# Kernel tuning notes

Measured on AMD Instinct MI355X. Metric: run time of the kernel, lower is better.

## Reference

```python
import jax, jax.numpy as jnp
import numpy as np

UNITS = 1024

def setup_inputs() -> dict:
    key = jax.random.key(0)
    k1, k2, k3 = jax.random.split(key, 3)
    B, T, F = 32, 512, 1024
    scale_g = 1.0 / np.sqrt(F + UNITS)
    return {
        "inputs": jax.random.normal(k1, (B, T, F), dtype=jnp.float32),
        "gate_kernel": jax.random.normal(k2, (F + UNITS, 2 * UNITS), dtype=jnp.float32) * scale_g,
        "gate_bias": jnp.ones((2 * UNITS,), dtype=jnp.float32),  # TF GRUCell default gate bias = 1.0
        "cand_kernel": jax.random.normal(k3, (F + UNITS, UNITS), dtype=jnp.float32) * scale_g,
        "cand_bias": jnp.zeros((UNITS,), dtype=jnp.float32),
    }

def _gru_step(x, h, gate_kernel, gate_bias, cand_kernel, cand_bias):
    # TF GRUCell math: gates from [x, h], candidate from [x, r*h]
    xh = jnp.concatenate([x, h], axis=-1)                      # [B, F+U]
    gates = jax.nn.sigmoid(xh @ gate_kernel + gate_bias)       # [B, 2U]
    r, u = jnp.split(gates, 2, axis=-1)
    xrh = jnp.concatenate([x, r * h], axis=-1)
    c = jnp.tanh(xrh @ cand_kernel + cand_bias)                # [B, U]
    return u * h + (1.0 - u) * c

def reference(inputs, gate_kernel, gate_bias, cand_kernel, cand_bias):
    B = inputs.shape[0]
    h0 = jnp.zeros((B, UNITS), dtype=jnp.float32)  # cell.zero_state
    xs = jnp.swapaxes(inputs, 0, 1)                # [T, B, F] (unstack over time)

    def step(h, x):
        h_new = _gru_step(x, h, gate_kernel, gate_bias, cand_kernel, cand_bias)
        return h_new, h_new  # GRU output == new state

    _, ys = jax.lax.scan(step, h0, xs)             # ys: [T, B, U]
    return jnp.swapaxes(ys, 0, 1)                  # stack on axis=1 -> [B, T, U]
```

## Files before the change

kernel.cpp:

```cpp
#include <hip/hip_runtime.h>
#include <math.h>

#define BB 32
#define TT 512
#define FF 1024
#define UU 1024

typedef __attribute__((ext_vector_type(8))) short s8v;
typedef __attribute__((ext_vector_type(4))) float f4v;

static __device__ __forceinline__ unsigned short f2bf(float f) {
    unsigned int u = __builtin_bit_cast(unsigned int, f);
    u += 0x7fff + ((u >> 16) & 1);
    return (unsigned short)(u >> 16);
}
static __device__ __forceinline__ float bf2f(unsigned short b) {
    unsigned int u = ((unsigned int)b) << 16;
    return __builtin_bit_cast(float, u);
}

__global__ __launch_bounds__(256) void cvt_bf16(
    const float* __restrict__ in, unsigned short* __restrict__ out, int n4)
{
    int i = blockIdx.x * 256 + threadIdx.x;
    if (i < n4) {
        float4 v = ((const float4*)in)[i];
        ushort4 o;
        o.x = f2bf(v.x); o.y = f2bf(v.y); o.z = f2bf(v.z); o.w = f2bf(v.w);
        ((ushort4*)out)[i] = o;
    }
}

template<int ROWS, int COLS>
__global__ __launch_bounds__(256) void transpose_bf16(
    const float* __restrict__ W, unsigned short* __restrict__ WT)
{
    __shared__ float tl[32][33];
    const int tx = threadIdx.x, ty = threadIdx.y;
    const int bx = blockIdx.x, by = blockIdx.y;
    #pragma unroll
    for (int i = 0; i < 4; ++i) {
        int r = by * 32 + ty + i * 8;
        int c = bx * 32 + tx;
        tl[ty + i * 8][tx] = W[(size_t)r * COLS + c];
    }
    __syncthreads();
    #pragma unroll
    for (int i = 0; i < 4; ++i) {
        int n = bx * 32 + ty + i * 8;
        int k = by * 32 + tx;
        WT[(size_t)n * ROWS + k] = f2bf(tl[tx][ty + i * 8]);
    }
}

__global__ __launch_bounds__(256) void gemm_xproj(
    const unsigned short* __restrict__ A,
    const unsigned short* __restrict__ BT,
    unsigned short* __restrict__ C,
    int N)
{
    __shared__ unsigned short Al[128][72];
    __shared__ unsigned short Bl[128][72];
    const int tid  = threadIdx.x;
    const int lane = tid & 63;
    const int wave = tid >> 6;
    const int l15  = lane & 15;
    const int kg   = lane >> 4;
    const int m0   = blockIdx.y * 128;
    const int n0   = blockIdx.x * 128;
    const int rowOff = (wave >> 1) * 64;
    const int colOff = (wave & 1) * 64;

    f4v acc[4][4];
    #pragma unroll
    for (int m = 0; m < 4; ++m)
        #pragma unroll
        for (int n = 0; n < 4; ++n) acc[m][n] = (f4v){0.f, 0.f, 0.f, 0.f};

    for (int k0 = 0; k0 < 1024; k0 += 64) {
        #pragma unroll
        for (int it = 0; it < 4; ++it) {
            int c = tid + it * 256;
            int r = c >> 3, off = (c & 7) * 8;
            *(s8v*)&Al[r][off] = *(const s8v*)(A + (size_t)(m0 + r) * 1024 + k0 + off);
            *(s8v*)&Bl[r][off] = *(const s8v*)(BT + (size_t)(n0 + r) * 2048 + k0 + off);
        }
        __syncthreads();
        #pragma unroll
        for (int ks = 0; ks < 2; ++ks) {
            s8v a[4], b[4];
            #pragma unroll
            for (int m = 0; m < 4; ++m)
                a[m] = *(const s8v*)&Al[rowOff + m * 16 + l15][ks * 32 + kg * 8];
            #pragma unroll
            for (int n = 0; n < 4; ++n)
                b[n] = *(const s8v*)&Bl[colOff + n * 16 + l15][ks * 32 + kg * 8];
            #pragma unroll
            for (int m = 0; m < 4; ++m)
                #pragma unroll
                for (int n = 0; n < 4; ++n)
                    acc[m][n] = __builtin_amdgcn_mfma_f32_16x16x32_bf16(a[m], b[n], acc[m][n], 0, 0, 0);
        }
        __syncthreads();
    }
    #pragma unroll
    for (int m = 0; m < 4; ++m)
        #pragma unroll
        for (int n = 0; n < 4; ++n)
            #pragma unroll
            for (int i = 0; i < 4; ++i) {
                int row = m0 + rowOff + m * 16 + kg * 4 + i;
                int col = n0 + colOff + n * 16 + l15;
                C[(size_t)row * N + col] = f2bf(acc[m][n][i]);
            }
}

__global__ __launch_bounds__(256) void gru_gates2(
    const unsigned short* __restrict__ hb,
    const unsigned short* __restrict__ WgT,
    const unsigned short* __restrict__ Xgb,
    const float* __restrict__ bg,
    const float* __restrict__ h,
    unsigned short* __restrict__ rhb,
    float* __restrict__ ubuf,
    int t)
{
    __shared__ unsigned short hb_l[32][1032];
    __shared__ unsigned short Wl[16][1032];
    __shared__ float red[4][32][16];
    const int tid  = threadIdx.x;
    const int lane = tid & 63;
    const int wave = tid >> 6;
    const int l15  = lane & 15;
    const int kg   = lane >> 4;
    const int j0   = blockIdx.x * 16;

    #pragma unroll
    for (int it = 0; it < 16; ++it) {
        int c = tid + it * 256;
        int r = c >> 7, off = (c & 127) * 8;
        *(s8v*)&hb_l[r][off] = *(const s8v*)(hb + (size_t)r * 1024 + off);
    }
    #pragma unroll
    for (int it = 0; it < 8; ++it) {
        int c = tid + it * 256;
        int r = c >> 7, off = (c & 127) * 8;
        *(s8v*)&Wl[r][off] = *(const s8v*)(WgT + (size_t)(j0 + r) * 2048 + 1024 + off);
    }
    __syncthreads();

    f4v acc0 = (f4v){0.f,0.f,0.f,0.f}, acc1 = (f4v){0.f,0.f,0.f,0.f};
    const int kbase = wave * 256;
    #pragma unroll
    for (int kk = 0; kk < 8; ++kk) {
        int k = kbase + kk * 32 + kg * 8;
        s8v a0 = *(const s8v*)&hb_l[l15][k];
        s8v a1 = *(const s8v*)&hb_l[16 + l15][k];
        s8v b  = *(const s8v*)&Wl[l15][k];
        acc0 = __builtin_amdgcn_mfma_f32_16x16x32_bf16(a0, b, acc0, 0, 0, 0);
        acc1 = __builtin_amdgcn_mfma_f32_16x16x32_bf16(a1, b, acc1, 0, 0, 0);
    }
    #pragma unroll
    for (int i = 0; i < 4; ++i) {
        red[wave][kg * 4 + i][l15]      = acc0[i];
        red[wave][16 + kg * 4 + i][l15] = acc1[i];
    }
    __syncthreads();

    for (int e = tid; e < 512; e += 256) {
        int b = e >> 4, col = e & 15;
        int j = j0 + col;
        float pre = red[0][b][col] + red[1][b][col] + red[2][b][col] + red[3][b][col];
        pre += bf2f(Xgb[((size_t)b * TT + t) * 2048 + j]) + bg[j];
        float s = 1.f / (1.f + __expf(-pre));
        if (j < UU) rhb[b * UU + j] = f2bf(s * h[b * UU + j]);
        else        ubuf[b * UU + (j - UU)] = s;
    }
}

__global__ __launch_bounds__(256) void gru_cand2(
    const unsigned short* __restrict__ rhb,
    const unsigned short* __restrict__ WcT,
    const unsigned short* __restrict__ Xcb,
    const float* __restrict__ bc,
    const float* __restrict__ ubuf,
    float* __restrict__ h,
    unsigned short* __restrict__ hb,
    float* __restrict__ out,
    int t)
{
    __shared__ unsigned short rh_l[32][1032];
    __shared__ unsigned short Wl[16][1032];
    __shared__ float red[4][32][16];
    const int tid  = threadIdx.x;
    const int lane = tid & 63;
    const int wave = tid >> 6;
    const int l15  = lane & 15;
    const int kg   = lane >> 4;
    const int j0   = blockIdx.x * 16;

    #pragma unroll
    for (int it = 0; it < 16; ++it) {
        int c = tid + it * 256;
        int r = c >> 7, off = (c & 127) * 8;
        *(s8v*)&rh_l[r][off] = *(const s8v*)(rhb + (size_t)r * 1024 + off);
    }
    #pragma unroll
    for (int it = 0; it < 8; ++it) {
        int c = tid + it * 256;
        int r = c >> 7, off = (c & 127) * 8;
        *(s8v*)&Wl[r][off] = *(const s8v*)(WcT + (size_t)(j0 + r) * 2048 + 1024 + off);
    }
    __syncthreads();

    f4v acc0 = (f4v){0.f,0.f,0.f,0.f}, acc1 = (f4v){0.f,0.f,0.f,0.f};
    const int kbase = wave * 256;
    #pragma unroll
    for (int kk = 0; kk < 8; ++kk) {
        int k = kbase + kk * 32 + kg * 8;
        s8v a0 = *(const s8v*)&rh_l[l15][k];
        s8v a1 = *(const s8v*)&rh_l[16 + l15][k];
        s8v b  = *(const s8v*)&Wl[l15][k];
        acc0 = __builtin_amdgcn_mfma_f32_16x16x32_bf16(a0, b, acc0, 0, 0, 0);
        acc1 = __builtin_amdgcn_mfma_f32_16x16x32_bf16(a1, b, acc1, 0, 0, 0);
    }
    #pragma unroll
    for (int i = 0; i < 4; ++i) {
        red[wave][kg * 4 + i][l15]      = acc0[i];
        red[wave][16 + kg * 4 + i][l15] = acc1[i];
    }
    __syncthreads();

    for (int e = tid; e < 512; e += 256) {
        int b = e >> 4, col = e & 15;
        int j = j0 + col;
        float pre = red[0][b][col] + red[1][b][col] + red[2][b][col] + red[3][b][col];
        pre += bf2f(Xcb[((size_t)b * TT + t) * 1024 + j]) + bc[j];
        float cv = tanhf(pre);
        float u  = ubuf[b * UU + j];
        float hv = h[b * UU + j];
        float hn = u * hv + (1.f - u) * cv;
        h[b * UU + j]  = hn;
        hb[b * UU + j] = f2bf(hn);
        out[((size_t)b * TT + t) * UU + j] = hn;
    }
}

__global__ __launch_bounds__(256) void gru_gates(
    const float* __restrict__ x, const float* __restrict__ Wg,
    const float* __restrict__ bg, const float* __restrict__ h,
    float* __restrict__ rh, float* __restrict__ ubuf, int t)
{
    __shared__ float xh[BB][64];
    __shared__ float wl[64][32];
    const int tid = threadIdx.x, jloc = tid & 31, b0 = (tid >> 5) * 4;
    const int j0 = blockIdx.x * 32;
    float acc0 = 0.f, acc1 = 0.f, acc2 = 0.f, acc3 = 0.f;
    for (int k0 = 0; k0 < FF + UU; k0 += 64) {
        for (int idx = tid; idx < BB * 64; idx += 256) {
            int b = idx >> 6, kk = idx & 63, k = k0 + kk;
            xh[b][kk] = (k < FF) ? x[(size_t)b * TT * FF + (size_t)t * FF + k]
                                 : h[b * UU + (k - FF)];
        }
        for (int idx = tid; idx < 64 * 32; idx += 256) {
            int kk = idx >> 5, jj = idx & 31;
            wl[kk][jj] = Wg[(size_t)(k0 + kk) * (2 * UU) + (j0 + jj)];
        }
        __syncthreads();
        #pragma unroll
        for (int kk = 0; kk < 64; kk += 4) {
            float w0 = wl[kk][jloc], w1 = wl[kk+1][jloc], w2 = wl[kk+2][jloc], w3 = wl[kk+3][jloc];
            float4 a0 = *(const float4*)&xh[b0+0][kk], a1 = *(const float4*)&xh[b0+1][kk];
            float4 a2 = *(const float4*)&xh[b0+2][kk], a3 = *(const float4*)&xh[b0+3][kk];
            acc0 += a0.x*w0 + a0.y*w1 + a0.z*w2 + a0.w*w3;
            acc1 += a1.x*w0 + a1.y*w1 + a1.z*w2 + a1.w*w3;
            acc2 += a2.x*w0 + a2.y*w1 + a2.z*w2 + a2.w*w3;
            acc3 += a3.x*w0 + a3.y*w1 + a3.z*w2 + a3.w*w3;
        }
        __syncthreads();
    }
    const int j = j0 + jloc;
    const float bias = bg[j];
    float g[4] = {acc0+bias, acc1+bias, acc2+bias, acc3+bias};
    #pragma unroll
    for (int i = 0; i < 4; ++i) {
        int b = b0 + i;
        float s = 1.f / (1.f + expf(-g[i]));
        if (j < UU) rh[b * UU + j] = s * h[b * UU + j];
        else        ubuf[b * UU + (j - UU)] = s;
    }
}

__global__ __launch_bounds__(256) void gru_cand(
    const float* __restrict__ x, const float* __restrict__ Wc,
    const float* __restrict__ bc, const float* __restrict__ rh,
    const float* __restrict__ ubuf, float* __restrict__ h,
    float* __restrict__ out, int t)
{
    __shared__ float xh[BB][64];
    __shared__ float wl[64][32];
    const int tid = threadIdx.x, jloc = tid & 31, b0 = (tid >> 5) * 4;
    const int j0 = blockIdx.x * 32;
    float acc0 = 0.f, acc1 = 0.f, acc2 = 0.f, acc3 = 0.f;
    for (int k0 = 0; k0 < FF + UU; k0 += 64) {
        for (int idx = tid; idx < BB * 64; idx += 256) {
            int b = idx >> 6, kk = idx & 63, k = k0 + kk;
            xh[b][kk] = (k < FF) ? x[(size_t)b * TT * FF + (size_t)t * FF + k]
                                 : rh[b * UU + (k - FF)];
        }
        for (int idx = tid; idx < 64 * 32; idx += 256) {
            int kk = idx >> 5, jj = idx & 31;
            wl[kk][jj] = Wc[(size_t)(k0 + kk) * UU + (j0 + jj)];
        }
        __syncthreads();
        #pragma unroll
        for (int kk = 0; kk < 64; kk += 4) {
            float w0 = wl[kk][jloc], w1 = wl[kk+1][jloc], w2 = wl[kk+2][jloc], w3 = wl[kk+3][jloc];
            float4 a0 = *(const float4*)&xh[b0+0][kk], a1 = *(const float4*)&xh[b0+1][kk];
            float4 a2 = *(const float4*)&xh[b0+2][kk], a3 = *(const float4*)&xh[b0+3][kk];
            acc0 += a0.x*w0 + a0.y*w1 + a0.z*w2 + a0.w*w3;
            acc1 += a1.x*w0 + a1.y*w1 + a1.z*w2 + a1.w*w3;
            acc2 += a2.x*w0 + a2.y*w1 + a2.z*w2 + a2.w*w3;
            acc3 += a3.x*w0 + a3.y*w1 + a3.z*w2 + a3.w*w3;
        }
        __syncthreads();
    }
    const int j = j0 + jloc;
    const float bias = bc[j];
    float cpre[4] = {acc0+bias, acc1+bias, acc2+bias, acc3+bias};
    #pragma unroll
    for (int i = 0; i < 4; ++i) {
        int b = b0 + i;
        float c  = tanhf(cpre[i]);
        float u  = ubuf[b * UU + j];
        float hv = h[b * UU + j];
        float hn = u * hv + (1.f - u) * c;
        h[b * UU + j] = hn;
        out[(size_t)b * TT * UU + (size_t)t * UU + j] = hn;
    }
}

extern "C" void kernel_launch(void* const* d_in, const int* in_sizes, int n_in,
                              void* d_out, int out_size, void* d_ws, size_t ws_size,
                              hipStream_t stream) {
    const float* x  = (const float*)d_in[0];
    const float* Wg = (const float*)d_in[1];
    const float* bg = (const float*)d_in[2];
    const float* Wc = (const float*)d_in[3];
    const float* bc = (const float*)d_in[4];
    float* out = (float*)d_out;

    const size_t XB_B  = (size_t)BB * TT * FF * 2;
    const size_t WGT_B = (size_t)2 * UU * (FF + UU) * 2;
    const size_t WCT_B = (size_t)UU * (FF + UU) * 2;
    const size_t XG_B  = (size_t)BB * TT * 2 * UU * 2;
    const size_t XC_B  = (size_t)BB * TT * UU * 2;
    const size_t H_B   = (size_t)BB * UU * 4;
    const size_t HB_B  = (size_t)BB * UU * 2;
    const size_t NEED  = XB_B + WGT_B + WCT_B + XG_B + XC_B + H_B + HB_B * 2 + H_B;

    if (ws_size >= NEED) {
        char* p = (char*)d_ws;
        unsigned short* xb  = (unsigned short*)p;            p += XB_B;
        unsigned short* WgT = (unsigned short*)p;            p += WGT_B;
        unsigned short* WcT = (unsigned short*)p;            p += WCT_B;
        unsigned short* Xgb = (unsigned short*)p;            p += XG_B;
        unsigned short* Xcb = (unsigned short*)p;            p += XC_B;
        float*          h   = (float*)p;                     p += H_B;
        unsigned short* hb  = (unsigned short*)p;            p += HB_B;
        unsigned short* rhb = (unsigned short*)p;            p += HB_B;
        float*          ub  = (float*)p;                     p += H_B;

        cvt_bf16<<<(BB * TT * FF / 4 + 255) / 256, 256, 0, stream>>>(x, xb, BB * TT * FF / 4);
        transpose_bf16<FF + UU, 2 * UU><<<dim3(64, 64), dim3(32, 8), 0, stream>>>(Wg, WgT);
        transpose_bf16<FF + UU, UU>    <<<dim3(32, 64), dim3(32, 8), 0, stream>>>(Wc, WcT);
        gemm_xproj<<<dim3(2 * UU / 128, BB * TT / 128), 256, 0, stream>>>(xb, WgT, Xgb, 2 * UU);
        gemm_xproj<<<dim3(UU / 128,     BB * TT / 128), 256, 0, stream>>>(xb, WcT, Xcb, UU);
        hipMemsetAsync(h,  0, H_B,  stream);
        hipMemsetAsync(hb, 0, HB_B, stream);

        for (int t = 0; t < TT; ++t) {
            gru_gates2<<<128, 256, 0, stream>>>(hb, WgT, Xgb, bg, h, rhb, ub, t);
            gru_cand2 <<< 64, 256, 0, stream>>>(rhb, WcT, Xcb, bc, ub, h, hb, out, t);
        }
    } else {
        float* h    = (float*)d_ws;
        float* rh   = h  + BB * UU;
        float* ubuf = rh + BB * UU;
        hipMemsetAsync(h, 0, BB * UU * sizeof(float), stream);
        for (int t = 0; t < TT; ++t) {
            gru_gates<<<64, 256, 0, stream>>>(x, Wg, bg, h, rh, ubuf, t);
            gru_cand <<<32, 256, 0, stream>>>(x, Wc, bc, rh, ubuf, h, out, t);
        }
    }
}
```

Measured before the change: 5.307 ms.

## Replace per-timestep kernel launches with persistent kernel using grid barriers

Fuses the gate and candidate recurrent kernels into one persistent kernel of 64 blocks that loops over all 512 timesteps, with an atomic-counter grid barrier between phases. Recurrent weight slices are held in registers across all timesteps instead of being reloaded into shared memory each launch. The aim is to remove about 1024 kernel launches and the repeated weight traffic. In exchange it relies on all 64 blocks being co-resident and spin-waits on global atomics. It also swaps tanhf for a clamped exp-based tanh and drops the fp32 fallback path.

```diff
diff --git a/kernel.cpp b/kernel.cpp
--- a/kernel.cpp
+++ b/kernel.cpp
@@ -5,6 +5,7 @@
 #define TT 512
 #define FF 1024
 #define UU 1024
+#define NBLK 64
 
 typedef __attribute__((ext_vector_type(8))) short s8v;
 typedef __attribute__((ext_vector_type(4))) float f4v;
@@ -115,40 +116,207 @@
             }
 }
 
-__global__ __launch_bounds__(256) void gru_gates2(
-    const unsigned short* __restrict__ hb,
+__device__ __forceinline__ void grid_barrier(unsigned* counter, unsigned* gen,
+                                             unsigned epoch, int tid)
+{
+    __syncthreads();
+    if (tid == 0) {
+        __threadfence();
+        unsigned arrived = __hip_atomic_fetch_add(counter, 1u, __ATOMIC_ACQ_REL,
+                                                  __HIP_MEMORY_SCOPE_AGENT);
+        if (arrived == NBLK - 1) {
+            __hip_atomic_store(counter, 0u, __ATOMIC_RELAXED, __HIP_MEMORY_SCOPE_AGENT);
+            __hip_atomic_store(gen, epoch, __ATOMIC_RELEASE, __HIP_MEMORY_SCOPE_AGENT);
+        } else {
+            while (__hip_atomic_load(gen, __ATOMIC_ACQUIRE, __HIP_MEMORY_SCOPE_AGENT) < epoch)
+                __builtin_amdgcn_s_sleep(1);
+        }
+    }
+    __syncthreads();
+}
+
+__global__ __launch_bounds__(256, 1) void gru_persistent(
     const unsigned short* __restrict__ WgT,
+    const unsigned short* __restrict__ WcT,
     const unsigned short* __restrict__ Xgb,
+    const unsigned short* __restrict__ Xcb,
     const float* __restrict__ bg,
-    const float* __restrict__ h,
+    const float* __restrict__ bc,
+    float* __restrict__ h,
+    unsigned short* __restrict__ hb,
     unsigned short* __restrict__ rhb,
-    float* __restrict__ ubuf,
-    int t)
-{
-    __shared__ unsigned short hb_l[32][1032];
-    __shared__ unsigned short Wl[16][1032];
-    __shared__ float red[4][32][16];
+    float* __restrict__ ub,
+    float* __restrict__ out,
+    unsigned* __restrict__ bar)
+{
+    __shared__ float red[4][32][32];
     const int tid  = threadIdx.x;
     const int lane = tid & 63;
     const int wave = tid >> 6;
     const int l15  = lane & 15;
     const int kg   = lane >> 4;
-    const int j0   = blockIdx.x * 16;
-
+    const int blk  = blockIdx.x;
+    const int gj0  = blk * 32;
+    const int cj0  = blk * 16;
+    const int kb   = wave * 256;
+    const bool is_r = (gj0 < UU);
+
+    s8v bgf[2][8], bcf[8];
+    #pragma unroll
+    for (int n = 0; n < 2; ++n)
+        #pragma unroll
+        for (int kk = 0; kk < 8; ++kk)
+            bgf[n][kk] = *(const s8v*)(WgT + (size_t)(gj0 + n * 16 + l15) * 2048
+                                            + 1024 + kb + kk * 32 + kg * 8);
+    #pragma unroll
+    for (int kk = 0; kk < 8; ++kk)
+        bcf[kk] = *(const s8v*)(WcT + (size_t)(cj0 + l15) * 2048
+                                     + 1024 + kb + kk * 32 + kg * 8);
+
+    const int eb = tid >> 3;
+    const int eq = tid & 7;
+    const float4 bgv = *(const float4*)(bg + gj0 + eq * 4);
+    const float2 bcv = *(const float2*)(bc + cj0 + eq * 2);
+
+    unsigned* counter = bar;
+    unsigned* gen     = bar + 1;
+    unsigned epoch = 0;
+
+    for (int t = 0; t < TT; ++t) {
+        ushort4 xg = *(const ushort4*)(Xgb + ((size_t)eb * TT + t) * 2048 + gj0 + eq * 4);
+        float4 hsl;
+        if (is_r) hsl = *(const float4*)(h + eb * UU + gj0 + eq * 4);
+
+        s8v a[2][8];
+        #pragma unroll
+        for (int m = 0; m < 2; ++m)
+            #pragma unroll
+            for (int kk = 0; kk < 8; ++kk)
+                a[m][kk] = *(const s8v*)(hb + (size_t)(m * 16 + l15) * 1024 + kb + kk * 32 + kg * 8);
+
+        f4v acc[2][2];
+        #pragma unroll
+        for (int m = 0; m < 2; ++m)
+            #pragma unroll
+            for (int n = 0; n < 2; ++n) acc[m][n] = (f4v){0.f, 0.f, 0.f, 0.f};
+        #pragma unroll
+        for (int kk = 0; kk < 8; ++kk)
+            #pragma unroll
+            for (int m = 0; m < 2; ++m)
+                #pragma unroll
+                for (int n = 0; n < 2; ++n)
+                    acc[m][n] = __builtin_amdgcn_mfma_f32_16x16x32_bf16(a[m][kk], bgf[n][kk], acc[m][n], 0, 0, 0);
+
+        #pragma unroll
+        for (int m = 0; m < 2; ++m)
+            #pragma unroll
+            for (int n = 0; n < 2; ++n)
+                #pragma unroll
+                for (int i = 0; i < 4; ++i)
+                    red[wave][m * 16 + kg * 4 + i][n * 16 + l15] = acc[m][n][i];
+        __syncthreads();
+
+        f4v pre = *(const f4v*)&red[0][eb][eq * 4];
+        #pragma unroll
+        for (int w = 1; w < 4; ++w) pre += *(const f4v*)&red[w][eb][eq * 4];
+        pre[0] += bf2f(xg.x) + bgv.x;
+        pre[1] += bf2f(xg.y) + bgv.y;
+        pre[2] += bf2f(xg.z) + bgv.z;
+        pre[3] += bf2f(xg.w) + bgv.w;
+        float s0 = 1.f / (1.f + __expf(-pre[0]));
+        float s1 = 1.f / (1.f + __expf(-pre[1]));
+        float s2 = 1.f / (1.f + __expf(-pre[2]));
+        float s3 = 1.f / (1.f + __expf(-pre[3]));
+        if (is_r) {
+            ushort4 o;
+            o.x = f2bf(s0 * hsl.x); o.y = f2bf(s1 * hsl.y);
+            o.z = f2bf(s2 * hsl.z); o.w = f2bf(s3 * hsl.w);
+            *(ushort4*)(rhb + eb * UU + gj0 + eq * 4) = o;
+        } else {
+            float4 uo = {s0, s1, s2, s3};
+            *(float4*)(ub + eb * UU + (gj0 - UU) + eq * 4) = uo;
+        }
+        ++epoch;
+        grid_barrier(counter, gen, epoch, tid);
+
+        ushort2 xc = *(const ushort2*)(Xcb + ((size_t)eb * TT + t) * 1024 + cj0 + eq * 2);
+        float2 uv  = *(const float2*)(ub + eb * UU + cj0 + eq * 2);
+        float2 hv  = *(const float2*)(h  + eb * UU + cj0 + eq * 2);
+
+        s8v ac[2][8];
+        #pragma unroll
+        for (int m = 0; m < 2; ++m)
+            #pragma unroll
+            for (int kk = 0; kk < 8; ++kk)
+                ac[m][kk] = *(const s8v*)(rhb + (size_t)(m * 16 + l15) * 1024 + kb + kk * 32 + kg * 8);
+
+        f4v acc2[2];
+        acc2[0] = (f4v){0.f, 0.f, 0.f, 0.f};
+        acc2[1] = (f4v){0.f, 0.f, 0.f, 0.f};
+        #pragma unroll
+        for (int kk = 0; kk < 8; ++kk)
+            #pragma unroll
+            for (int m = 0; m < 2; ++m)
+                acc2[m] = __builtin_amdgcn_mfma_f32_16x16x32_bf16(ac[m][kk], bcf[kk], acc2[m], 0, 0, 0);
+
+        float* redc = (float*)red;
+        __syncthreads();
+        #pragma unroll
+        for (int m = 0; m < 2; ++m)
+            #pragma unroll
+            for (int i = 0; i < 4; ++i)
+                redc[((size_t)wave * 32 + m * 16 + kg * 4 + i) * 16 + l15] = acc2[m][i];
+        __syncthreads();
+
+        float2 pre2 = *(const float2*)&redc[(0 * 32 + eb) * 16 + eq * 2];
+        #pragma unroll
+        for (int w = 1; w < 4; ++w) {
+            float2 p = *(const float2*)&redc[((size_t)w * 32 + eb) * 16 + eq * 2];
+            pre2.x += p.x; pre2.y += p.y;
+        }
+        float c0 = pre2.x + bf2f(xc.x) + bcv.x;
+        float c1 = pre2.y + bf2f(xc.y) + bcv.y;
+        c0 = fminf(fmaxf(c0, -15.f), 15.f);
+        c1 = fminf(fmaxf(c1, -15.f), 15.f);
+        float e0 = __expf(2.f * c0), e1 = __expf(2.f * c1);
+        float t0 = (e0 - 1.f) / (e0 + 1.f);
+        float t1 = (e1 - 1.f) / (e1 + 1.f);
+        float hn0 = uv.x * hv.x + (1.f - uv.x) * t0;
+        float hn1 = uv.y * hv.y + (1.f - uv.y) * t1;
+
+        *(float2*)(h + eb * UU + cj0 + eq * 2) = make_float2(hn0, hn1);
+        ushort2 hbo; hbo.x = f2bf(hn0); hbo.y = f2bf(hn1);
+        *(ushort2*)(hb + eb * UU + cj0 + eq * 2) = hbo;
+        *(float2*)(out + ((size_t)eb * TT + t) * UU + cj0 + eq * 2) = make_float2(hn0, hn1);
+
+        ++epoch;
+        grid_barrier(counter, gen, epoch, tid);
+    }
+}
+
+__global__ __launch_bounds__(256) void gru_gates2(
+    const unsigned short* __restrict__ hb, const unsigned short* __restrict__ WgT,
+    const unsigned short* __restrict__ Xgb, const float* __restrict__ bg,
+    const float* __restrict__ h, unsigned short* __restrict__ rhb,
+    float* __restrict__ ubuf, int t)
+{
+    __shared__ unsigned short hb_l[32][1032];
+    __shared__ unsigned short Wl[16][1032];
+    __shared__ float red[4][32][16];
+    const int tid = threadIdx.x, lane = tid & 63, wave = tid >> 6;
+    const int l15 = lane & 15, kg = lane >> 4;
+    const int j0 = blockIdx.x * 16;
     #pragma unroll
     for (int it = 0; it < 16; ++it) {
-        int c = tid + it * 256;
-        int r = c >> 7, off = (c & 127) * 8;
+        int c = tid + it * 256; int r = c >> 7, off = (c & 127) * 8;
         *(s8v*)&hb_l[r][off] = *(const s8v*)(hb + (size_t)r * 1024 + off);
     }
     #pragma unroll
     for (int it = 0; it < 8; ++it) {
-        int c = tid + it * 256;
-        int r = c >> 7, off = (c & 127) * 8;
+        int c = tid + it * 256; int r = c >> 7, off = (c & 127) * 8;
         *(s8v*)&Wl[r][off] = *(const s8v*)(WgT + (size_t)(j0 + r) * 2048 + 1024 + off);
     }
     __syncthreads();
-
     f4v acc0 = (f4v){0.f,0.f,0.f,0.f}, acc1 = (f4v){0.f,0.f,0.f,0.f};
     const int kbase = wave * 256;
     #pragma unroll
@@ -162,11 +330,10 @@
     }
     #pragma unroll
     for (int i = 0; i < 4; ++i) {
-        red[wave][kg * 4 + i][l15]      = acc0[i];
+        red[wave][kg * 4 + i][l15] = acc0[i];
         red[wave][16 + kg * 4 + i][l15] = acc1[i];
     }
     __syncthreads();
-
     for (int e = tid; e < 512; e += 256) {
         int b = e >> 4, col = e & 15;
         int j = j0 + col;
@@ -179,40 +346,28 @@
 }
 
 __global__ __launch_bounds__(256) void gru_cand2(
-    const unsigned short* __restrict__ rhb,
-    const unsigned short* __restrict__ WcT,
-    const unsigned short* __restrict__ Xcb,
-    const float* __restrict__ bc,
-    const float* __restrict__ ubuf,
-    float* __restrict__ h,
-    unsigned short* __restrict__ hb,
-    float* __restrict__ out,
-    int t)
+    const unsigned short* __restrict__ rhb, const unsigned short* __restrict__ WcT,
+    const unsigned short* __restrict__ Xcb, const float* __restrict__ bc,
+    const float* __restrict__ ubuf, float* __restrict__ h,
+    unsigned short* __restrict__ hb, float* __restrict__ out, int t)
 {
     __shared__ unsigned short rh_l[32][1032];
     __shared__ unsigned short Wl[16][1032];
     __shared__ float red[4][32][16];
-    const int tid  = threadIdx.x;
-    const int lane = tid & 63;
-    const int wave = tid >> 6;
-    const int l15  = lane & 15;
-    const int kg   = lane >> 4;
-    const int j0   = blockIdx.x * 16;
-
+    const int tid = threadIdx.x, lane = tid & 63, wave = tid >> 6;
+    const int l15 = lane & 15, kg = lane >> 4;
+    const int j0 = blockIdx.x * 16;
     #pragma unroll
     for (int it = 0; it < 16; ++it) {
-        int c = tid + it * 256;
-        int r = c >> 7, off = (c & 127) * 8;
+        int c = tid + it * 256; int r = c >> 7, off = (c & 127) * 8;
         *(s8v*)&rh_l[r][off] = *(const s8v*)(rhb + (size_t)r * 1024 + off);
     }
     #pragma unroll
     for (int it = 0; it < 8; ++it) {
-        int c = tid + it * 256;
-        int r = c >> 7, off = (c & 127) * 8;
+        int c = tid + it * 256; int r = c >> 7, off = (c & 127) * 8;
         *(s8v*)&Wl[r][off] = *(const s8v*)(WcT + (size_t)(j0 + r) * 2048 + 1024 + off);
     }
     __syncthreads();
-
     f4v acc0 = (f4v){0.f,0.f,0.f,0.f}, acc1 = (f4v){0.f,0.f,0.f,0.f};
     const int kbase = wave * 256;
     #pragma unroll
@@ -226,11 +381,10 @@
     }
     #pragma unroll
     for (int i = 0; i < 4; ++i) {
-        red[wave][kg * 4 + i][l15]      = acc0[i];
+        red[wave][kg * 4 + i][l15] = acc0[i];
         red[wave][16 + kg * 4 + i][l15] = acc1[i];
     }
     __syncthreads();
-
     for (int e = tid; e < 512; e += 256) {
         int b = e >> 4, col = e & 15;
         int j = j0 + col;
@@ -246,100 +400,6 @@
     }
 }
 
-__global__ __launch_bounds__(256) void gru_gates(
-    const float* __restrict__ x, const float* __restrict__ Wg,
-    const float* __restrict__ bg, const float* __restrict__ h,
-    float* __restrict__ rh, float* __restrict__ ubuf, int t)
-{
-    __shared__ float xh[BB][64];
-    __shared__ float wl[64][32];
-    const int tid = threadIdx.x, jloc = tid & 31, b0 = (tid >> 5) * 4;
-    const int j0 = blockIdx.x * 32;
-    float acc0 = 0.f, acc1 = 0.f, acc2 = 0.f, acc3 = 0.f;
-    for (int k0 = 0; k0 < FF + UU; k0 += 64) {
-        for (int idx = tid; idx < BB * 64; idx += 256) {
-            int b = idx >> 6, kk = idx & 63, k = k0 + kk;
-            xh[b][kk] = (k < FF) ? x[(size_t)b * TT * FF + (size_t)t * FF + k]
-                                 : h[b * UU + (k - FF)];
-        }
-        for (int idx = tid; idx < 64 * 32; idx += 256) {
-            int kk = idx >> 5, jj = idx & 31;
-            wl[kk][jj] = Wg[(size_t)(k0 + kk) * (2 * UU) + (j0 + jj)];
-        }
-        __syncthreads();
-        #pragma unroll
-        for (int kk = 0; kk < 64; kk += 4) {
-            float w0 = wl[kk][jloc], w1 = wl[kk+1][jloc], w2 = wl[kk+2][jloc], w3 = wl[kk+3][jloc];
-            float4 a0 = *(const float4*)&xh[b0+0][kk], a1 = *(const float4*)&xh[b0+1][kk];
-            float4 a2 = *(const float4*)&xh[b0+2][kk], a3 = *(const float4*)&xh[b0+3][kk];
-            acc0 += a0.x*w0 + a0.y*w1 + a0.z*w2 + a0.w*w3;
-            acc1 += a1.x*w0 + a1.y*w1 + a1.z*w2 + a1.w*w3;
-            acc2 += a2.x*w0 + a2.y*w1 + a2.z*w2 + a2.w*w3;
-            acc3 += a3.x*w0 + a3.y*w1 + a3.z*w2 + a3.w*w3;
-        }
-        __syncthreads();
-    }
-    const int j = j0 + jloc;
-    const float bias = bg[j];
-    float g[4] = {acc0+bias, acc1+bias, acc2+bias, acc3+bias};
-    #pragma unroll
-    for (int i = 0; i < 4; ++i) {
-        int b = b0 + i;
-        float s = 1.f / (1.f + expf(-g[i]));
-        if (j < UU) rh[b * UU + j] = s * h[b * UU + j];
-        else        ubuf[b * UU + (j - UU)] = s;
-    }
-}
-
-__global__ __launch_bounds__(256) void gru_cand(
-    const float* __restrict__ x, const float* __restrict__ Wc,
-    const float* __restrict__ bc, const float* __restrict__ rh,
-    const float* __restrict__ ubuf, float* __restrict__ h,
-    float* __restrict__ out, int t)
-{
-    __shared__ float xh[BB][64];
-    __shared__ float wl[64][32];
-    const int tid = threadIdx.x, jloc = tid & 31, b0 = (tid >> 5) * 4;
-    const int j0 = blockIdx.x * 32;
-    float acc0 = 0.f, acc1 = 0.f, acc2 = 0.f, acc3 = 0.f;
-    for (int k0 = 0; k0 < FF + UU; k0 += 64) {
-        for (int idx = tid; idx < BB * 64; idx += 256) {
-            int b = idx >> 6, kk = idx & 63, k = k0 + kk;
-            xh[b][kk] = (k < FF) ? x[(size_t)b * TT * FF + (size_t)t * FF + k]
-                                 : rh[b * UU + (k - FF)];
-        }
-        for (int idx = tid; idx < 64 * 32; idx += 256) {
-            int kk = idx >> 5, jj = idx & 31;
-            wl[kk][jj] = Wc[(size_t)(k0 + kk) * UU + (j0 + jj)];
-        }
-        __syncthreads();
-        #pragma unroll
-        for (int kk = 0; kk < 64; kk += 4) {
-            float w0 = wl[kk][jloc], w1 = wl[kk+1][jloc], w2 = wl[kk+2][jloc], w3 = wl[kk+3][jloc];
-            float4 a0 = *(const float4*)&xh[b0+0][kk], a1 = *(const float4*)&xh[b0+1][kk];
-            float4 a2 = *(const float4*)&xh[b0+2][kk], a3 = *(const float4*)&xh[b0+3][kk];
-            acc0 += a0.x*w0 + a0.y*w1 + a0.z*w2 + a0.w*w3;
-            acc1 += a1.x*w0 + a1.y*w1 + a1.z*w2 + a1.w*w3;
-            acc2 += a2.x*w0 + a2.y*w1 + a2.z*w2 + a2.w*w3;
-            acc3 += a3.x*w0 + a3.y*w1 + a3.z*w2 + a3.w*w3;
-        }
-        __syncthreads();
-    }
-    const int j = j0 + jloc;
-    const float bias = bc[j];
-    float cpre[4] = {acc0+bias, acc1+bias, acc2+bias, acc3+bias};
-    #pragma unroll
-    for (int i = 0; i < 4; ++i) {
-        int b = b0 + i;
-        float c  = tanhf(cpre[i]);
-        float u  = ubuf[b * UU + j];
-        float hv = h[b * UU + j];
-        float hn = u * hv + (1.f - u) * c;
-        h[b * UU + j] = hn;
-        out[(size_t)b * TT * UU + (size_t)t * UU + j] = hn;
-    }
-}
-
 extern "C" void kernel_launch(void* const* d_in, const int* in_sizes, int n_in,
                               void* d_out, int out_size, void* d_ws, size_t ws_size,
                               hipStream_t stream) {
@@ -357,40 +417,37 @@
     const size_t XC_B  = (size_t)BB * TT * UU * 2;
     const size_t H_B   = (size_t)BB * UU * 4;
     const size_t HB_B  = (size_t)BB * UU * 2;
-    const size_t NEED  = XB_B + WGT_B + WCT_B + XG_B + XC_B + H_B + HB_B * 2 + H_B;
+    const size_t BAR_B = 256;
+    const size_t NEED  = XB_B + WGT_B + WCT_B + XG_B + XC_B + H_B + HB_B * 2 + H_B + BAR_B;
+
+    char* p = (char*)d_ws;
+    unsigned short* xb  = (unsigned short*)p;            p += XB_B;
+    unsigned short* WgT = (unsigned short*)p;            p += WGT_B;
+    unsigned short* WcT = (unsigned short*)p;            p += WCT_B;
+    unsigned short* Xgb = (unsigned short*)p;            p += XG_B;
+    unsigned short* Xcb = (unsigned short*)p;            p += XC_B;
+    float*          h   = (float*)p;                     p += H_B;
+    unsigned short* hb  = (unsigned short*)p;            p += HB_B;
+    unsigned short* rhb = (unsigned short*)p;            p += HB_B;
+    float*          ub  = (float*)p;                     p += H_B;
+    unsigned*       bar = (unsigned*)p;                  p += BAR_B;
+
+    cvt_bf16<<<(BB * TT * FF / 4 + 255) / 256, 256, 0, stream>>>(x, xb, BB * TT * FF / 4);
+    transpose_bf16<FF + UU, 2 * UU><<<dim3(64, 64), dim3(32, 8), 0, stream>>>(Wg, WgT);
+    transpose_bf16<FF + UU, UU>    <<<dim3(32, 64), dim3(32, 8), 0, stream>>>(Wc, WcT);
+    gemm_xproj<<<dim3(2 * UU / 128, BB * TT / 128), 256, 0, stream>>>(xb, WgT, Xgb, 2 * UU);
+    gemm_xproj<<<dim3(UU / 128,     BB * TT / 128), 256, 0, stream>>>(xb, WcT, Xcb, UU);
+    hipMemsetAsync(h,   0, H_B,   stream);
+    hipMemsetAsync(hb,  0, HB_B,  stream);
+    hipMemsetAsync(bar, 0, BAR_B, stream);
 
     if (ws_size >= NEED) {
-        char* p = (char*)d_ws;
-        unsigned short* xb  = (unsigned short*)p;            p += XB_B;
-        unsigned short* WgT = (unsigned short*)p;            p += WGT_B;
-        unsigned short* WcT = (unsigned short*)p;            p += WCT_B;
-        unsigned short* Xgb = (unsigned short*)p;            p += XG_B;
-        unsigned short* Xcb = (unsigned short*)p;            p += XC_B;
-        float*          h   = (float*)p;                     p += H_B;
-        unsigned short* hb  = (unsigned short*)p;            p += HB_B;
-        unsigned short* rhb = (unsigned short*)p;            p += HB_B;
-        float*          ub  = (float*)p;                     p += H_B;
-
-        cvt_bf16<<<(BB * TT * FF / 4 + 255) / 256, 256, 0, stream>>>(x, xb, BB * TT * FF / 4);
-        transpose_bf16<FF + UU, 2 * UU><<<dim3(64, 64), dim3(32, 8), 0, stream>>>(Wg, WgT);
-        transpose_bf16<FF + UU, UU>    <<<dim3(32, 64), dim3(32, 8), 0, stream>>>(Wc, WcT);
-        gemm_xproj<<<dim3(2 * UU / 128, BB * TT / 128), 256, 0, stream>>>(xb, WgT, Xgb, 2 * UU);
-        gemm_xproj<<<dim3(UU / 128,     BB * TT / 128), 256, 0, stream>>>(xb, WcT, Xcb, UU);
-        hipMemsetAsync(h,  0, H_B,  stream);
-        hipMemsetAsync(hb, 0, HB_B, stream);
-
+        gru_persistent<<<NBLK, 256, 0, stream>>>(WgT, WcT, Xgb, Xcb, bg, bc,
+                                                 h, hb, rhb, ub, out, bar);
+    } else {
         for (int t = 0; t < TT; ++t) {
             gru_gates2<<<128, 256, 0, stream>>>(hb, WgT, Xgb, bg, h, rhb, ub, t);
             gru_cand2 <<< 64, 256, 0, stream>>>(rhb, WcT, Xcb, bc, ub, h, hb, out, t);
         }
-    } else {
-        float* h    = (float*)d_ws;
-        float* rh   = h  + BB * UU;
-        float* ubuf = rh + BB * UU;
-        hipMemsetAsync(h, 0, BB * UU * sizeof(float), stream);
-        for (int t = 0; t < TT; ++t) {
-            gru_gates<<<64, 256, 0, stream>>>(x, Wg, bg, h, rh, ubuf, t);
-            gru_cand <<<32, 256, 0, stream>>>(x, Wc, bc, rh, ubuf, h, out, t);
-        }
-    }
-}
+    }
+}
```

After: 9.692 ms. 1.83x slower.
